# Kernel optimization log

Measured on AMD Instinct MI355X. Metric: run time of the kernel, lower is better.

## Reference

```python
import jax, jax.numpy as jnp
import numpy as np
from jax import lax

V, E, HD, B, S, T = 50000, 256, 512, 32, 256, 24
H = HD // 2  # per-direction hidden size


def setup_inputs() -> dict:
    key = jax.random.key(0)
    ks = jax.random.split(key, 15)
    def n(k, shape, scale=0.1):
        return jax.random.normal(k, shape, jnp.float32) * scale
    return dict(
        sentence=jax.random.randint(ks[0], (B, S), 0, V),
        embed=n(ks[1], (V, E)),
        Wih_f=n(ks[2], (4 * H, E)), Whh_f=n(ks[3], (4 * H, H)),
        bih_f=n(ks[4], (4 * H,)), bhh_f=n(ks[5], (4 * H,)),
        Wih_b=n(ks[6], (4 * H, E)), Whh_b=n(ks[7], (4 * H, H)),
        bih_b=n(ks[8], (4 * H,)), bhh_b=n(ks[9], (4 * H,)),
        Wout=n(ks[10], (T, HD)), bout=n(ks[11], (T,)),
        transitions=n(ks[12], (T, T), 1.0),
        start_t=n(ks[13], (T,), 1.0),
        stop_t=n(ks[14], (T,), 1.0),
    )


def _lstm_dir(xs, Wih, Whh, bih, bhh, reverse):
    # xs: [S, B, E] -> hs: [S, B, H]; PyTorch gate order i,f,g,o
    bsz, hh = xs.shape[1], Whh.shape[1]
    x_proj = jnp.einsum('sbe,ge->sbg', xs, Wih) + bih + bhh  # [S,B,4H]
    def step(carry, xp):
        h, c = carry
        gates = xp + h @ Whh.T
        i, f, g, o = jnp.split(gates, 4, axis=-1)
        c = jax.nn.sigmoid(f) * c + jax.nn.sigmoid(i) * jnp.tanh(g)
        h = jax.nn.sigmoid(o) * jnp.tanh(c)
        return (h, c), h
    init = (jnp.zeros((bsz, hh), xs.dtype), jnp.zeros((bsz, hh), xs.dtype))
    _, hs = lax.scan(step, init, x_proj, reverse=reverse)
    return hs


def _features(sentence, embed, Wih_f, Whh_f, bih_f, bhh_f,
              Wih_b, Whh_b, bih_b, bhh_b, Wout, bout):
    emb = embed[sentence]                      # [B,S,E]
    xs = jnp.swapaxes(emb, 0, 1)               # [S,B,E]
    hf = _lstm_dir(xs, Wih_f, Whh_f, bih_f, bhh_f, reverse=False)
    hb = _lstm_dir(xs, Wih_b, Whh_b, bih_b, bhh_b, reverse=True)
    hs = jnp.concatenate([hf, hb], axis=-1)    # [S,B,HD]
    return jnp.einsum('sbh,th->sbt', hs, Wout) + bout  # [S,B,T]


def reference(sentence, embed, Wih_f, Whh_f, bih_f, bhh_f,
              Wih_b, Whh_b, bih_b, bhh_b, Wout, bout,
              transitions, start_t, stop_t):
    feats = _features(sentence, embed, Wih_f, Whh_f, bih_f, bhh_f,
                      Wih_b, Whh_b, bih_b, bhh_b, Wout, bout)  # [S,B,T]
    # Viterbi decode (faithful to _viterbi_decode)
    v0 = feats[0] + start_t[None, :]           # [B,T]
    def step(v, feat):
        scores = v[:, :, None] + transitions[None]  # [B, prev T, next T]
        idx = jnp.argmax(scores, axis=1)       # [B,T] best previous tag
        v = jnp.max(scores, axis=1) + feat
        return v, idx
    v, idxs = lax.scan(step, v0, feats[1:])    # idxs: [S-1,B,T]
    last = jnp.argmax(v + stop_t[None, :], axis=1)  # [B]
    def back(tag, idx):
        tag = jnp.take_along_axis(idx, tag[:, None], axis=1)[:, 0]
        return tag, tag
    _, prev_tags = lax.scan(back, last, idxs, reverse=True)  # [S-1,B]
    tags = jnp.concatenate([prev_tags, last[None]], axis=0)  # [S,B]
    return jnp.swapaxes(tags, 0, 1)            # [B,S]
```

## Files before the change

kernel.cpp:

```cpp
#include <hip/hip_runtime.h>
#include <hip/hip_bf16.h>


#define S_LEN 256
#define BATCH 32
#define NTAG  24

__global__ __launch_bounds__(256) void k_prep(
    const float* __restrict__ WhhF, const float* __restrict__ WhhB,
    float* __restrict__ Wt) {
  int idx = blockIdx.x * 256 + threadIdx.x;
  int dir = idx >> 18;
  int r = idx & 262143;
  int k = r >> 10;
  int jg = r & 1023;
  int j = jg >> 2, g = jg & 3;
  const float* W = dir ? WhhB : WhhF;
  Wt[idx] = W[(size_t)(g * 256 + j) * 256 + k];
}

__global__ __launch_bounds__(256) void k_inproj(
    const int* __restrict__ sent, const float* __restrict__ embed,
    const float* __restrict__ WihF, const float* __restrict__ bihF, const float* __restrict__ bhhF,
    const float* __restrict__ WihB, const float* __restrict__ bihB, const float* __restrict__ bhhB,
    float* __restrict__ xq) {
  int tm = blockIdx.x;
  int tn = blockIdx.y;
  int dir = blockIdx.z;
  const float* Wih = dir ? WihB : WihF;
  const float* bih = dir ? bihB : bihF;
  const float* bhh = dir ? bhhB : bhhF;
  __shared__ float As[64 * 36];
  __shared__ float Bs[64 * 36];
  __shared__ int toks[64];
  int tid = threadIdx.x;
  if (tid < 64) {
    int r = tm * 64 + tid;
    int s = r >> 5, b = r & 31;
    toks[tid] = sent[b * S_LEN + s];
  }
  __syncthreads();
  int mt = tid & 15, nt = tid >> 4;
  float acc[4][4] = {};
  for (int k0 = 0; k0 < 256; k0 += 32) {
    for (int it = 0; it < 2; ++it) {
      int u = it * 256 + tid;
      int row = u >> 3, lf = u & 7;
      float4 av = *(const float4*)&embed[(size_t)toks[row] * 256 + k0 + lf * 4];
      *(float4*)&As[row * 36 + lf * 4] = av;
      int grow = tn * 64 + row;
      float4 wv = *(const float4*)&Wih[(size_t)grow * 256 + k0 + lf * 4];
      *(float4*)&Bs[row * 36 + lf * 4] = wv;
    }
    __syncthreads();
#pragma unroll
    for (int kc = 0; kc < 8; ++kc) {
      float4 a[4], w[4];
#pragma unroll
      for (int i = 0; i < 4; ++i) a[i] = *(const float4*)&As[(mt + 16 * i) * 36 + kc * 4];
#pragma unroll
      for (int j = 0; j < 4; ++j) w[j] = *(const float4*)&Bs[(nt + 16 * j) * 36 + kc * 4];
#pragma unroll
      for (int i = 0; i < 4; ++i)
#pragma unroll
        for (int j = 0; j < 4; ++j)
          acc[i][j] += a[i].x * w[j].x + a[i].y * w[j].y + a[i].z * w[j].z + a[i].w * w[j].w;
    }
    __syncthreads();
  }
#pragma unroll
  for (int i = 0; i < 4; ++i) {
    int r = tm * 64 + mt + 16 * i;
    int s = r >> 5, b = r & 31;
#pragma unroll
    for (int j = 0; j < 4; ++j) {
      int gg = tn * 64 + nt + 16 * j;
      float v = acc[i][j] + bih[gg] + bhh[gg];
      xq[(((size_t)(dir * 32 + b)) * 256 + s) * 1024 + (gg & 255) * 4 + (gg >> 8)] = v;
    }
  }
}

__global__ __launch_bounds__(256, 1) void k_lstm(
    const float* __restrict__ Wt,
    const float* __restrict__ xq,
    unsigned long long* __restrict__ hX2,
    float* __restrict__ hsF) {
  int B = blockIdx.x;
  int q = (B >> 3) & 3;
  int gid = (B & 7) | ((B >> 5) << 3);
  int dir = gid >> 5;
  int b = gid & 31;
  int tid = threadIdx.x;
  int w = tid >> 6;
  int l = tid & 63;
  int kbase = w * 64;
  int unit = q * 64 + l;

  __shared__ float red[4][64 * 8];

  float4 wreg[64];
  {
    const float* wp = Wt + ((size_t)dir * 256 + kbase) * 1024 + unit * 4;
#pragma unroll
    for (int kk = 0; kk < 64; ++kk)
      wreg[kk] = *(const float4*)(wp + (size_t)kk * 1024);
  }

  float c_st = 0.f;

#pragma unroll 1
  for (int t = 0; t < 256; ++t) {
    int s = dir ? (255 - t) : t;

    float4 xv = {0.f, 0.f, 0.f, 0.f};
    if (w == 0)
      xv = *(const float4*)&xq[(((size_t)(dir * 32 + b)) * 256 + s) * 1024 + unit * 4];

    float hval;
    {
      const unsigned long long* hp =
          hX2 + ((((size_t)(t & 1) * 2 + dir) * 32 + b) * 256 + kbase + l);
      unsigned long long a;
      unsigned spins = 0;
      while (true) {
        a = __hip_atomic_load(hp, __ATOMIC_RELAXED, __HIP_MEMORY_SCOPE_AGENT);
        if (__all((unsigned)(a >> 32) == (unsigned)t)) break;
        if (++spins > (1u << 18)) break;
      }
      hval = __uint_as_float((unsigned)a);
    }

    float4 acc = {0.f, 0.f, 0.f, 0.f};
#pragma unroll
    for (int kk = 0; kk < 64; ++kk) {
      float hk = __shfl(hval, kk);
      acc.x += wreg[kk].x * hk;
      acc.y += wreg[kk].y * hk;
      acc.z += wreg[kk].z * hk;
      acc.w += wreg[kk].w * hk;
    }
    *(float4*)&red[w][l * 8] = acc;
    __syncthreads();

    if (w == 0) {
      float4 r0 = *(const float4*)&red[0][l * 8];
      float4 r1 = *(const float4*)&red[1][l * 8];
      float4 r2 = *(const float4*)&red[2][l * 8];
      float4 r3 = *(const float4*)&red[3][l * 8];
      float xi = r0.x + r1.x + r2.x + r3.x + xv.x;
      float xf = r0.y + r1.y + r2.y + r3.y + xv.y;
      float xg = r0.z + r1.z + r2.z + r3.z + xv.z;
      float xo = r0.w + r1.w + r2.w + r3.w + xv.w;
      float si = 1.f / (1.f + expf(-xi));
      float sf = 1.f / (1.f + expf(-xf));
      float so = 1.f / (1.f + expf(-xo));
      float tg = tanhf(xg);
      c_st = sf * c_st + si * tg;
      float h = so * tanhf(c_st);
      unsigned long long atom =
          ((unsigned long long)(unsigned)(t + 1) << 32) |
          (unsigned long long)__float_as_uint(h);
      unsigned long long* hn =
          hX2 + ((((size_t)((t + 1) & 1) * 2 + dir) * 32 + b) * 256 + unit);
      __hip_atomic_store(hn, atom, __ATOMIC_RELAXED, __HIP_MEMORY_SCOPE_AGENT);
      hsF[(((size_t)(dir * 32 + b)) * 256 + s) * 256 + unit] = h;
    }
  }
}

__global__ __launch_bounds__(256) void k_feats(
    const float* __restrict__ hsF, const float* __restrict__ Wout,
    const float* __restrict__ bout, float* __restrict__ feats) {
  int s = blockIdx.x;
  int tid = threadIdx.x;
  __shared__ float Hl[32 * 260];
  __shared__ float Wl[24 * 260];
  float acc[3] = {};
  for (int dir = 0; dir < 2; ++dir) {
    __syncthreads();
    for (int u = tid; u < 8192; u += 256) {
      int b = u >> 8, j = u & 255;
      Hl[b * 260 + j] = hsF[(((size_t)(dir * 32 + b)) * 256 + s) * 256 + j];
    }
    for (int u = tid; u < 24 * 256; u += 256) {
      int t = u >> 8, j = u & 255;
      Wl[t * 260 + j] = Wout[t * 512 + dir * 256 + j];
    }
    __syncthreads();
    int b = tid & 31, th = tid >> 5;
    for (int jc = 0; jc < 64; ++jc) {
      float4 hv = *(const float4*)&Hl[b * 260 + jc * 4];
#pragma unroll
      for (int rep = 0; rep < 3; ++rep) {
        int t = rep * 8 + th;
        float4 wv = *(const float4*)&Wl[t * 260 + jc * 4];
        acc[rep] += hv.x * wv.x + hv.y * wv.y + hv.z * wv.z + hv.w * wv.w;
      }
    }
  }
  int b = tid & 31, th = tid >> 5;
#pragma unroll
  for (int rep = 0; rep < 3; ++rep) {
    int t = rep * 8 + th;
    feats[((size_t)s * 32 + b) * 24 + t] = acc[rep] + bout[t];
  }
}

__global__ __launch_bounds__(64) void k_viterbi(
    const float* __restrict__ feats, const float* __restrict__ trans,
    const float* __restrict__ start_t, const float* __restrict__ stop_t,
    int* __restrict__ out) {
  int b = blockIdx.x;
  int j = threadIdx.x;
  bool act = j < NTAG;
  int j2 = act ? j : 0;
  __shared__ unsigned char idxL[255 * 24];
  __shared__ float sv[32];
  float tr[24];
#pragma unroll
  for (int i = 0; i < 24; ++i) tr[i] = trans[i * 24 + j2];
  float vj = feats[(size_t)b * 24 + j2] + start_t[j2];
  if (!act) vj = -1e30f;
#pragma unroll 1
  for (int s = 1; s < 256; ++s) {
    float m = -1e30f;
    int arg = 0;
#pragma unroll
    for (int i = 0; i < 24; ++i) {
      float vi = __shfl(vj, i);
      float sc = vi + tr[i];
      if (sc > m) { m = sc; arg = i; }
    }
    float fj = feats[((size_t)s * 32 + b) * 24 + j2];
    if (act) {
      idxL[(s - 1) * 24 + j] = (unsigned char)arg;
      vj = m + fj;
    }
  }
  if (act) sv[j] = vj + stop_t[j];
  __syncthreads();
  if (j == 0) {
    float m = sv[0];
    int tag = 0;
    for (int i = 1; i < 24; ++i)
      if (sv[i] > m) { m = sv[i]; tag = i; }
    out[b * 256 + 255] = tag;
    for (int s = 254; s >= 0; --s) {
      tag = idxL[s * 24 + tag];
      out[b * 256 + s] = tag;
    }
  }
}

extern "C" void kernel_launch(void* const* d_in, const int* in_sizes, int n_in,
                              void* d_out, int out_size, void* d_ws, size_t ws_size,
                              hipStream_t stream) {
  const int*   sent   = (const int*)  d_in[0];
  const float* embed  = (const float*)d_in[1];
  const float* WihF   = (const float*)d_in[2];
  const float* WhhF   = (const float*)d_in[3];
  const float* bihF   = (const float*)d_in[4];
  const float* bhhF   = (const float*)d_in[5];
  const float* WihB   = (const float*)d_in[6];
  const float* WhhB   = (const float*)d_in[7];
  const float* bihB   = (const float*)d_in[8];
  const float* bhhB   = (const float*)d_in[9];
  const float* Wout   = (const float*)d_in[10];
  const float* bout   = (const float*)d_in[11];
  const float* trans  = (const float*)d_in[12];
  const float* startt = (const float*)d_in[13];
  const float* stopt  = (const float*)d_in[14];
  int* out = (int*)d_out;

  char* ws = (char*)d_ws;
  size_t off = 0;
  float* xq = (float*)(ws + off);           off += (size_t)2 * 32 * 256 * 1024 * 4;
  size_t off_sync = off;
  unsigned long long* hX2 = (unsigned long long*)(ws + off);
                                            off += (size_t)2 * 2 * 32 * 256 * 8;
  size_t sync_len = off - off_sync;
  float* hsF = (float*)(ws + off);          off += (size_t)2 * 32 * 256 * 256 * 4;
  float* feats = (float*)(ws + off);        off += (size_t)256 * 32 * 24 * 4;
  float* Wt = (float*)(ws + off);           off += (size_t)2 * 256 * 1024 * 4;

  hipMemsetAsync(ws + off_sync, 0, sync_len, stream);

  k_prep<<<2048, 256, 0, stream>>>(WhhF, WhhB, Wt);
  k_inproj<<<dim3(128, 16, 2), 256, 0, stream>>>(sent, embed, WihF, bihF, bhhF,
                                                 WihB, bihB, bhhB, xq);
  k_lstm<<<256, 256, 0, stream>>>(Wt, xq, hX2, hsF);
  k_feats<<<256, 256, 0, stream>>>(hsF, Wout, bout, feats);
  k_viterbi<<<32, 64, 0, stream>>>(feats, trans, startt, stopt, out);
}
```

Baseline: 1.128 ms.

## Replace LDS reduction with in-wave shuffle reduction and prefetch next-step h/x

The LSTM recurrence kernel now assigns each of 4 adjacent lanes a quarter of the K dimension for one hidden unit. Partial sums are combined with xor shuffles, which removes the shared-memory reduction and __syncthreads from every timestep. Each lane polls four consecutive h flags. The next step's h values and x projection are loaded speculatively right after the matvec, so the spin-wait often finds them already present. It also switches to fast __expf-based sigmoid/tanh and shortens the spin timeout, at some cost in precision and in robustness of the timeout fallback.

```diff
diff --git a/kernel.cpp b/kernel.cpp
--- a/kernel.cpp
+++ b/kernel.cpp
@@ -5,6 +5,8 @@
 #define S_LEN 256
 #define BATCH 32
 #define NTAG  24
+
+typedef unsigned long long ull;
 
 __global__ __launch_bounds__(256) void k_prep(
     const float* __restrict__ WhhF, const float* __restrict__ WhhB,
@@ -84,7 +86,7 @@
 __global__ __launch_bounds__(256, 1) void k_lstm(
     const float* __restrict__ Wt,
     const float* __restrict__ xq,
-    unsigned long long* __restrict__ hX2,
+    ull* __restrict__ hX2,
     float* __restrict__ hsF) {
   int B = blockIdx.x;
   int q = (B >> 3) & 3;
@@ -92,80 +94,112 @@
   int dir = gid >> 5;
   int b = gid & 31;
   int tid = threadIdx.x;
-  int w = tid >> 6;
+  int u = tid >> 2;
+  int ks = tid & 3;
   int l = tid & 63;
-  int kbase = w * 64;
-  int unit = q * 64 + l;
-
-  __shared__ float red[4][64 * 8];
+  int unit = q * 64 + u;
+  int srcBase = ks * 16;
 
   float4 wreg[64];
   {
-    const float* wp = Wt + ((size_t)dir * 256 + kbase) * 1024 + unit * 4;
-#pragma unroll
-    for (int kk = 0; kk < 64; ++kk)
-      wreg[kk] = *(const float4*)(wp + (size_t)kk * 1024);
-  }
-
+    const float* wp = Wt + ((size_t)dir * 256 + ks * 64) * 1024 + unit * 4;
+#pragma unroll
+    for (int j = 0; j < 64; ++j)
+      wreg[j] = *(const float4*)(wp + (size_t)j * 1024);
+  }
+
+  const size_t grp = ((size_t)dir * 32 + b) * 256;
+  const size_t PARSZ = (size_t)2 * 32 * 256;
   float c_st = 0.f;
+
+  ull p0, p1, p2, p3;
+  {
+    const ull* hp = hX2 + (grp + 4 * l);
+    p0 = __hip_atomic_load(hp + 0, __ATOMIC_RELAXED, __HIP_MEMORY_SCOPE_AGENT);
+    p1 = __hip_atomic_load(hp + 1, __ATOMIC_RELAXED, __HIP_MEMORY_SCOPE_AGENT);
+    p2 = __hip_atomic_load(hp + 2, __ATOMIC_RELAXED, __HIP_MEMORY_SCOPE_AGENT);
+    p3 = __hip_atomic_load(hp + 3, __ATOMIC_RELAXED, __HIP_MEMORY_SCOPE_AGENT);
+  }
+  float4 xv = {0.f, 0.f, 0.f, 0.f};
+  if (ks == 0) {
+    int s0 = dir ? 255 : 0;
+    xv = *(const float4*)&xq[(((size_t)(dir * 32 + b)) * 256 + s0) * 1024 + unit * 4];
+  }
 
 #pragma unroll 1
   for (int t = 0; t < 256; ++t) {
     int s = dir ? (255 - t) : t;
-
-    float4 xv = {0.f, 0.f, 0.f, 0.f};
-    if (w == 0)
-      xv = *(const float4*)&xq[(((size_t)(dir * 32 + b)) * 256 + s) * 1024 + unit * 4];
-
-    float hval;
+    unsigned tgt = (unsigned)t;
+
     {
-      const unsigned long long* hp =
-          hX2 + ((((size_t)(t & 1) * 2 + dir) * 32 + b) * 256 + kbase + l);
-      unsigned long long a;
+      const ull* hp = hX2 + ((size_t)(t & 1) * PARSZ + grp + 4 * l);
       unsigned spins = 0;
       while (true) {
-        a = __hip_atomic_load(hp, __ATOMIC_RELAXED, __HIP_MEMORY_SCOPE_AGENT);
-        if (__all((unsigned)(a >> 32) == (unsigned)t)) break;
-        if (++spins > (1u << 18)) break;
+        bool ok = ((unsigned)(p0 >> 32) == tgt) & ((unsigned)(p1 >> 32) == tgt) &
+                  ((unsigned)(p2 >> 32) == tgt) & ((unsigned)(p3 >> 32) == tgt);
+        if (__all(ok)) break;
+        p0 = __hip_atomic_load(hp + 0, __ATOMIC_RELAXED, __HIP_MEMORY_SCOPE_AGENT);
+        p1 = __hip_atomic_load(hp + 1, __ATOMIC_RELAXED, __HIP_MEMORY_SCOPE_AGENT);
+        p2 = __hip_atomic_load(hp + 2, __ATOMIC_RELAXED, __HIP_MEMORY_SCOPE_AGENT);
+        p3 = __hip_atomic_load(hp + 3, __ATOMIC_RELAXED, __HIP_MEMORY_SCOPE_AGENT);
+        if (++spins > (1u << 14)) break;
       }
-      hval = __uint_as_float((unsigned)a);
-    }
+    }
+    float hpv[4];
+    hpv[0] = __uint_as_float((unsigned)p0);
+    hpv[1] = __uint_as_float((unsigned)p1);
+    hpv[2] = __uint_as_float((unsigned)p2);
+    hpv[3] = __uint_as_float((unsigned)p3);
 
     float4 acc = {0.f, 0.f, 0.f, 0.f};
 #pragma unroll
-    for (int kk = 0; kk < 64; ++kk) {
-      float hk = __shfl(hval, kk);
-      acc.x += wreg[kk].x * hk;
-      acc.y += wreg[kk].y * hk;
-      acc.z += wreg[kk].z * hk;
-      acc.w += wreg[kk].w * hk;
-    }
-    *(float4*)&red[w][l * 8] = acc;
-    __syncthreads();
-
-    if (w == 0) {
-      float4 r0 = *(const float4*)&red[0][l * 8];
-      float4 r1 = *(const float4*)&red[1][l * 8];
-      float4 r2 = *(const float4*)&red[2][l * 8];
-      float4 r3 = *(const float4*)&red[3][l * 8];
-      float xi = r0.x + r1.x + r2.x + r3.x + xv.x;
-      float xf = r0.y + r1.y + r2.y + r3.y + xv.y;
-      float xg = r0.z + r1.z + r2.z + r3.z + xv.z;
-      float xo = r0.w + r1.w + r2.w + r3.w + xv.w;
-      float si = 1.f / (1.f + expf(-xi));
-      float sf = 1.f / (1.f + expf(-xf));
-      float so = 1.f / (1.f + expf(-xo));
-      float tg = tanhf(xg);
-      c_st = sf * c_st + si * tg;
-      float h = so * tanhf(c_st);
-      unsigned long long atom =
-          ((unsigned long long)(unsigned)(t + 1) << 32) |
-          (unsigned long long)__float_as_uint(h);
-      unsigned long long* hn =
-          hX2 + ((((size_t)((t + 1) & 1) * 2 + dir) * 32 + b) * 256 + unit);
+    for (int j = 0; j < 64; ++j) {
+      float hk = __shfl(hpv[j & 3], srcBase + (j >> 2));
+      acc.x += wreg[j].x * hk;
+      acc.y += wreg[j].y * hk;
+      acc.z += wreg[j].z * hk;
+      acc.w += wreg[j].w * hk;
+    }
+    acc.x += __shfl_xor(acc.x, 1); acc.y += __shfl_xor(acc.y, 1);
+    acc.z += __shfl_xor(acc.z, 1); acc.w += __shfl_xor(acc.w, 1);
+    acc.x += __shfl_xor(acc.x, 2); acc.y += __shfl_xor(acc.y, 2);
+    acc.z += __shfl_xor(acc.z, 2); acc.w += __shfl_xor(acc.w, 2);
+
+    int tn = (t < 255) ? (t + 1) : 255;
+    {
+      const ull* hpn = hX2 + ((size_t)((t + 1) & 1) * PARSZ + grp + 4 * l);
+      p0 = __hip_atomic_load(hpn + 0, __ATOMIC_RELAXED, __HIP_MEMORY_SCOPE_AGENT);
+      p1 = __hip_atomic_load(hpn + 1, __ATOMIC_RELAXED, __HIP_MEMORY_SCOPE_AGENT);
+      p2 = __hip_atomic_load(hpn + 2, __ATOMIC_RELAXED, __HIP_MEMORY_SCOPE_AGENT);
+      p3 = __hip_atomic_load(hpn + 3, __ATOMIC_RELAXED, __HIP_MEMORY_SCOPE_AGENT);
+    }
+    float4 xvn = {0.f, 0.f, 0.f, 0.f};
+    if (ks == 0) {
+      int sn = dir ? (255 - tn) : tn;
+      xvn = *(const float4*)&xq[(((size_t)(dir * 32 + b)) * 256 + sn) * 1024 + unit * 4];
+    }
+
+    if (ks == 0) {
+      float xi = acc.x + xv.x;
+      float xf = acc.y + xv.y;
+      float xg = acc.z + xv.z;
+      float xo = acc.w + xv.w;
+      float si = 1.f / (1.f + __expf(-xi));
+      float sf = 1.f / (1.f + __expf(-xf));
+      float so = 1.f / (1.f + __expf(-xo));
+      float eg = __expf(-2.f * fabsf(xg));
+      float tg = __builtin_copysignf((1.f - eg) / (1.f + eg), xg);
+      float c = sf * c_st + si * tg;
+      c_st = c;
+      float ec = __expf(-2.f * fabsf(c));
+      float th = __builtin_copysignf((1.f - ec) / (1.f + ec), c);
+      float h = so * th;
+      ull atom = ((ull)(unsigned)(t + 1) << 32) | (ull)__float_as_uint(h);
+      ull* hn = hX2 + ((size_t)((t + 1) & 1) * PARSZ + grp + unit);
       __hip_atomic_store(hn, atom, __ATOMIC_RELAXED, __HIP_MEMORY_SCOPE_AGENT);
-      hsF[(((size_t)(dir * 32 + b)) * 256 + s) * 256 + unit] = h;
-    }
+      hsF[(grp + unit) * 0 + (((size_t)(dir * 32 + b)) * 256 + s) * 256 + unit] = h;
+    }
+    xv = xvn;
   }
 }
 
@@ -277,8 +311,7 @@
   size_t off = 0;
   float* xq = (float*)(ws + off);           off += (size_t)2 * 32 * 256 * 1024 * 4;
   size_t off_sync = off;
-  unsigned long long* hX2 = (unsigned long long*)(ws + off);
-                                            off += (size_t)2 * 2 * 32 * 256 * 8;
+  ull* hX2 = (ull*)(ws + off);              off += (size_t)2 * 2 * 32 * 256 * 8;
   size_t sync_len = off - off_sync;
   float* hsF = (float*)(ws + off);          off += (size_t)2 * 32 * 256 * 256 * 4;
   float* feats = (float*)(ws + off);        off += (size_t)256 * 32 * 24 * 4;
```

New measurement: 1.355 ms. +20.2%, slower.
